# Kernel optimization log

Measured on AMD Instinct MI355X. Metric: run time of the kernel, lower is better.

The kernel has to match this reference:

```python
import jax, jax.numpy as jnp
import numpy as np

N = 100000   # source points
M = 100000   # query (also) points
E = 2000000  # radius-neighbor pairs (row: query idx, col: source idx)
FEAT = 64
OUT = 2


def _linear_params(key, fan_in, fan_out):
    kw, kb = jax.random.split(key)
    bound = 1.0 / np.sqrt(fan_in)
    w = jax.random.uniform(kw, (fan_in, fan_out), jnp.float32, -bound, bound)
    b = jax.random.uniform(kb, (fan_out,), jnp.float32, -bound, bound)
    return w, b


def setup_inputs() -> dict:
    key = jax.random.key(0)
    ks = jax.random.split(key, 10)
    pcd = jax.random.normal(ks[0], (N, 3), jnp.float32)
    feats = jax.random.normal(ks[1], (N, FEAT), jnp.float32)
    also_pts = jax.random.normal(ks[2], (M, 3), jnp.float32)
    also_labels = jax.random.randint(ks[3], (M,), 0, 2, jnp.int64)
    row = jax.random.randint(ks[4], (E,), 0, M, jnp.int64)
    col = jax.random.randint(ks[5], (E,), 0, N, jnp.int64)
    w_in, b_in = _linear_params(ks[6], FEAT + 3, FEAT)
    w1, b1 = _linear_params(ks[7], FEAT, FEAT)
    w2, b2 = _linear_params(ks[8], FEAT, FEAT)
    w_out, b_out = _linear_params(ks[9], FEAT, OUT)
    return {"pcd": pcd, "feats": feats, "also_pts": also_pts,
            "also_labels": also_labels, "row": row, "col": col,
            "w_in": w_in, "b_in": b_in, "w1": w1, "b1": b1,
            "w2": w2, "b2": b2, "w_out": w_out, "b_out": b_out}


def reference(pcd, feats, also_pts, also_labels, row, col,
              w_in, b_in, w1, b1, w2, b2, w_out, b_out):
    # gather: relative position of query vs neighbor, and neighbor latent
    pos_relative = also_pts[row] - pcd[col]          # (E, 3)
    latents_relative = feats[col]                    # (E, FEAT)
    x = jnp.concatenate([latents_relative, pos_relative], axis=1)  # (E, FEAT+3)
    x = x @ w_in + b_in                              # fc_in
    x = jax.nn.relu(x) @ w1 + b1                     # mlp layer 0 (act then linear)
    x = jax.nn.relu(x) @ w2 + b2                     # mlp layer 1
    x = x @ w_out + b_out                            # fc_out -> (E, 2)
    probs = jax.nn.softmax(x, axis=1)
    return probs, also_labels[row]
```

## Files before the change

### kernel.cpp

```cpp
#include <hip/hip_runtime.h>
#include <hip/hip_bf16.h>


typedef _Float16 half8 __attribute__((ext_vector_type(8)));
typedef _Float16 half2v __attribute__((ext_vector_type(2)));
typedef __fp16   fp16x2 __attribute__((ext_vector_type(2)));
typedef __attribute__((ext_vector_type(4))) float f32x4;

union U84h { uint4 u; half8 h; };
union UPH  { half2v h; fp16x2 f; int i; unsigned u; };

__device__ __forceinline__ half2v cvt2h(float a, float b) {
    UPH t;
    t.f = __builtin_amdgcn_cvt_pkrtz(a, b);
    return t.h;
}

__device__ __forceinline__ half8 relu8(half8 v) {
    half8 z;
#pragma unroll
    for (int i = 0; i < 8; ++i) z[i] = (_Float16)0.f;
    return __builtin_elementwise_max(v, z);
}

__global__ __launch_bounds__(256) void pack_fold(
    const float* __restrict__ w1, const float* __restrict__ w_in,
    const float* __restrict__ b1, const float* __restrict__ w2,
    const float* __restrict__ w_out, const float* __restrict__ b2,
    const float* __restrict__ b_out,
    _Float16* __restrict__ w1f, _Float16* __restrict__ wAf,
    _Float16* __restrict__ wpf, _Float16* __restrict__ w0h,
    _Float16* __restrict__ w1h, _Float16* __restrict__ b1h,
    float* __restrict__ bf) {
    int t = blockIdx.x * 256 + threadIdx.x;
    if (t < 4096) {
        int f = t >> 9, lane = (t >> 3) & 63, j = t & 7;
        int ntile = f >> 1, kstep = f & 1;
        int k = kstep * 32 + ((lane >> 4) << 3) + j;
        int n = ntile * 16 + (lane & 15);
        w1f[t] = (_Float16)w1[k * 64 + n];
    } else if (t < 10240) {
        int i = t - 4096;
        int f = i >> 9, lane = (i >> 3) & 63, j = i & 7;
        int ntile = f / 3, ks = f % 3;
        int n = ntile * 16 + (lane & 15);
        float v;
        if (ks < 2) {
            int k = ks * 32 + ((lane >> 4) << 3) + j;
            v = w_in[k * 64 + n];
        } else {
            v = ((lane >> 4) == 0 && j < 3) ? -w_in[(64 + j) * 64 + n] : 0.f;
        }
        wAf[i] = (_Float16)v;
    } else if (t < 13312) {
        int i = t - 10240;
        int d = i >> 10, ks = (i >> 9) & 1, lane = (i >> 3) & 63, j = i & 7;
        int k = ks * 32 + ((lane >> 4) << 3) + j;
        wpf[i] = (_Float16)w_in[(64 + d) * 64 + k];
    } else if (t < 13376) {
        int n = t - 13312;
        float s0 = 0.f, s1 = 0.f;
#pragma unroll
        for (int j = 0; j < 64; ++j) {
            s0 = fmaf(w2[n * 64 + j], w_out[j * 2 + 0], s0);
            s1 = fmaf(w2[n * 64 + j], w_out[j * 2 + 1], s1);
        }
        w0h[n] = (_Float16)s0;
        w1h[n] = (_Float16)s1;
    } else if (t < 13440) {
        int n = t - 13376;
        b1h[n] = (_Float16)b1[n];
    } else if (t == 13440) {
        float s0 = b_out[0], s1 = b_out[1];
#pragma unroll
        for (int j = 0; j < 64; ++j) {
            s0 = fmaf(b2[j], w_out[j * 2 + 0], s0);
            s1 = fmaf(b2[j], w_out[j * 2 + 1], s1);
        }
        bf[0] = s0; bf[1] = s1;
    }
}

__global__ __launch_bounds__(256) void precompute_S(
    const float* __restrict__ feats, const float* __restrict__ pcd,
    const float* __restrict__ b_in, const half8* __restrict__ wAf,
    _Float16* __restrict__ S, int N) {
    int lane = threadIdx.x & 63;
    int idx = lane & 15, g = lane >> 4;
    int base = (blockIdx.x * 4 + (threadIdx.x >> 6)) * 16;
    if (base >= N) return;

    half8 wa[12];
#pragma unroll
    for (int f = 0; f < 12; ++f) wa[f] = wAf[f * 64 + lane];

    int p = base + idx;
    int ps = p < N ? p : N - 1;
    const float4* fp = (const float4*)(feats + (size_t)ps * 64);
    float4 f0 = fp[2 * g], f1 = fp[2 * g + 1];
    float4 f2 = fp[8 + 2 * g], f3 = fp[8 + 2 * g + 1];
    half8 b0, b1v, b2v;
    b0[0]=(_Float16)f0.x; b0[1]=(_Float16)f0.y; b0[2]=(_Float16)f0.z; b0[3]=(_Float16)f0.w;
    b0[4]=(_Float16)f1.x; b0[5]=(_Float16)f1.y; b0[6]=(_Float16)f1.z; b0[7]=(_Float16)f1.w;
    b1v[0]=(_Float16)f2.x; b1v[1]=(_Float16)f2.y; b1v[2]=(_Float16)f2.z; b1v[3]=(_Float16)f2.w;
    b1v[4]=(_Float16)f3.x; b1v[5]=(_Float16)f3.y; b1v[6]=(_Float16)f3.z; b1v[7]=(_Float16)f3.w;
    float px = 0.f, py = 0.f, pz = 0.f;
    if (g == 0) {
        const float* pp = pcd + (size_t)ps * 3;
        px = pp[0]; py = pp[1]; pz = pp[2];
    }
#pragma unroll
    for (int i = 0; i < 8; ++i) b2v[i] = (_Float16)0.f;
    b2v[0] = (_Float16)px; b2v[1] = (_Float16)py; b2v[2] = (_Float16)pz;

#pragma unroll
    for (int tt = 0; tt < 4; ++tt) {
        f32x4 bi = *(const f32x4*)(b_in + tt * 16 + 4 * g);
        f32x4 acc;
        acc = __builtin_amdgcn_mfma_f32_16x16x32_f16(wa[tt * 3 + 0], b0, bi, 0, 0, 0);
        acc = __builtin_amdgcn_mfma_f32_16x16x32_f16(wa[tt * 3 + 1], b1v, acc, 0, 0, 0);
        acc = __builtin_amdgcn_mfma_f32_16x16x32_f16(wa[tt * 3 + 2], b2v, acc, 0, 0, 0);
        union { uint2 u; _Float16 h[4]; } o;
        o.h[0] = (_Float16)acc[0]; o.h[1] = (_Float16)acc[1];
        o.h[2] = (_Float16)acc[2]; o.h[3] = (_Float16)acc[3];
        if (p < N) *(uint2*)(S + (size_t)p * 64 + tt * 16 + 4 * g) = o.u;
    }
}

__global__ __launch_bounds__(256, 4) void edge_mfma(
    const _Float16* __restrict__ S, const float* __restrict__ also_pts,
    const int* __restrict__ row, const int* __restrict__ col,
    const int* __restrict__ labels,
    const half8* __restrict__ w1f, const half8* __restrict__ wpf,
    const unsigned* __restrict__ w0p, const unsigned* __restrict__ w1p,
    const unsigned* __restrict__ b1p, const float* __restrict__ bfold,
    float* __restrict__ out, int E, int ngroups) {
    __shared__ half8 wf_lds[8][64];
    {
        int t = threadIdx.x;
        wf_lds[t >> 6][t & 63] = w1f[t];
        wf_lds[(t + 256) >> 6][t & 63] = w1f[t + 256];
    }
    __syncthreads();

    int lane = threadIdx.x & 63;
    int idx  = lane & 15;
    int g    = lane >> 4;
    int gwave  = blockIdx.x * 4 + (threadIdx.x >> 6);
    int nwaves = gridDim.x * 4;
    if (gwave >= ngroups) return;

    half8 wpd[3][2];
#pragma unroll
    for (int d = 0; d < 3; ++d)
#pragma unroll
        for (int ks = 0; ks < 2; ++ks) wpd[d][ks] = wpf[(d * 2 + ks) * 64 + lane];
    UPH w0v[8], w1v[8], b1v[8];
#pragma unroll
    for (int tt = 0; tt < 4; ++tt)
#pragma unroll
        for (int h = 0; h < 2; ++h) {
            int i = tt * 8 + 2 * g + h;
            w0v[tt * 2 + h].u = w0p[i];
            w1v[tt * 2 + h].u = w1p[i];
            b1v[tt * 2 + h].u = b1p[i];
        }
    float bf0 = bfold[0], bf1 = bfold[1];
    half2v zero2 = {(_Float16)0.f, (_Float16)0.f};

    int grp = gwave, stride = nwaves;
    int es0 = (grp << 4) + idx; es0 = es0 < E ? es0 : E - 1;
    int r_c = row[es0], c_c = col[es0];
    const uint4* sp0 = (const uint4*)(S + (size_t)c_c * 64);
    uint4 s0_c = sp0[g], s1_c = sp0[4 + g];
    const float* ap0 = also_pts + (size_t)r_c * 3;
    float ax_c = ap0[0], ay_c = ap0[1], az_c = ap0[2];
    int lb_c = labels[r_c];

    int gn = grp + stride; gn = gn < ngroups ? gn : grp;
    int es1 = (gn << 4) + idx; es1 = es1 < E ? es1 : E - 1;
    int r_n = row[es1], c_n = col[es1];

    for (; grp < ngroups; grp += stride) {
        const uint4* spn = (const uint4*)(S + (size_t)c_n * 64);
        uint4 s0_n = spn[g], s1_n = spn[4 + g];
        const float* apn = also_pts + (size_t)r_n * 3;
        float ax_n = apn[0], ay_n = apn[1], az_n = apn[2];
        int lb_n = labels[r_n];
        int g2 = grp + 2 * stride; g2 = g2 < ngroups ? g2 : grp;
        int es2 = (g2 << 4) + idx; es2 = es2 < E ? es2 : E - 1;
        int r_2 = row[es2], c_2 = col[es2];

        int e = (grp << 4) + idx;
        bool eok = e < E;
        U84h s0u, s1u; s0u.u = s0_c; s1u.u = s1_c;
        _Float16 ah = (_Float16)ax_c, bh = (_Float16)ay_c, ch = (_Float16)az_c;
        half8 av = {ah, ah, ah, ah, ah, ah, ah, ah};
        half8 bv = {bh, bh, bh, bh, bh, bh, bh, bh};
        half8 cv = {ch, ch, ch, ch, ch, ch, ch, ch};
        half8 q0 = av * wpd[0][0] + bv * wpd[1][0] + cv * wpd[2][0];
        half8 q1 = av * wpd[0][1] + bv * wpd[1][1] + cv * wpd[2][1];
        half8 x0 = relu8(s0u.h + q0);
        half8 x1 = relu8(s1u.h + q1);

        f32x4 zero = {0.f, 0.f, 0.f, 0.f};
        f32x4 acc[4];
#pragma unroll
        for (int tt = 0; tt < 4; ++tt) {
            acc[tt] = __builtin_amdgcn_mfma_f32_16x16x32_f16(wf_lds[2 * tt][lane],     x0, zero, 0, 0, 0);
            acc[tt] = __builtin_amdgcn_mfma_f32_16x16x32_f16(wf_lds[2 * tt + 1][lane], x1, acc[tt], 0, 0, 0);
        }

        half2v p0 = zero2, p1 = zero2;
#pragma unroll
        for (int tt = 0; tt < 4; ++tt) {
            half2v h01 = cvt2h(acc[tt][0], acc[tt][1]);
            half2v h23 = cvt2h(acc[tt][2], acc[tt][3]);
            h01 = __builtin_elementwise_max(h01 + b1v[tt * 2 + 0].h, zero2);
            h23 = __builtin_elementwise_max(h23 + b1v[tt * 2 + 1].h, zero2);
            p0 += h01 * w0v[tt * 2 + 0].h + h23 * w0v[tt * 2 + 1].h;
            p1 += h01 * w1v[tt * 2 + 0].h + h23 * w1v[tt * 2 + 1].h;
        }
        UPH P0, P1, T;
        P0.h = p0; P1.h = p1;
        T.i = __shfl_xor(P0.i, 16); P0.h += T.h;
        T.i = __shfl_xor(P0.i, 32); P0.h += T.h;
        T.i = __shfl_xor(P1.i, 16); P1.h += T.h;
        T.i = __shfl_xor(P1.i, 32); P1.h += T.h;

        if (g == 0 && eok) {
            float l0 = (float)P0.h[0] + (float)P0.h[1] + bf0;
            float l1 = (float)P1.h[0] + (float)P1.h[1] + bf1;
            float mx = fmaxf(l0, l1);
            float e0 = __expf(l0 - mx);
            float e1 = __expf(l1 - mx);
            float inv = 1.f / (e0 + e1);
            *(float2*)(out + (size_t)e * 2) = make_float2(e0 * inv, e1 * inv);
            out[(size_t)2 * E + e] = (float)lb_c;
        }

        s0_c = s0_n; s1_c = s1_n;
        ax_c = ax_n; ay_c = ay_n; az_c = az_n;
        lb_c = lb_n;
        r_n = r_2; c_n = c_2;
    }
}

extern "C" void kernel_launch(void* const* d_in, const int* in_sizes, int n_in,
                              void* d_out, int out_size, void* d_ws, size_t ws_size,
                              hipStream_t stream) {
    const float* pcd      = (const float*)d_in[0];
    const float* feats    = (const float*)d_in[1];
    const float* also_pts = (const float*)d_in[2];
    const int*   labels   = (const int*)d_in[3];
    const int*   row      = (const int*)d_in[4];
    const int*   col      = (const int*)d_in[5];
    const float* w_in     = (const float*)d_in[6];
    const float* b_in     = (const float*)d_in[7];
    const float* w1       = (const float*)d_in[8];
    const float* b1       = (const float*)d_in[9];
    const float* w2       = (const float*)d_in[10];
    const float* b2       = (const float*)d_in[11];
    const float* w_out    = (const float*)d_in[12];
    const float* b_out    = (const float*)d_in[13];

    int N = in_sizes[0] / 3;
    int E = in_sizes[4];

    _Float16* Sb  = (_Float16*)d_ws;
    _Float16* w1f = Sb + (size_t)N * 64;
    _Float16* wAf = w1f + 4096;
    _Float16* wpf = wAf + 6144;
    _Float16* w0h = wpf + 3072;
    _Float16* w1h = w0h + 64;
    _Float16* b1h = w1h + 64;
    float*    bf  = (float*)(b1h + 64);

    pack_fold<<<53, 256, 0, stream>>>(w1, w_in, b1, w2, w_out, b2, b_out,
                                      w1f, wAf, wpf, w0h, w1h, b1h, bf);

    int ngroupsS = (N + 15) / 16;
    precompute_S<<<(ngroupsS + 3) / 4, 256, 0, stream>>>(
        feats, pcd, b_in, (const half8*)wAf, Sb, N);

    int ngroups = (E + 15) / 16;
    edge_mfma<<<2048, 256, 0, stream>>>(Sb, also_pts, row, col, labels,
                                        (const half8*)w1f, (const half8*)wpf,
                                        (const unsigned*)w0h, (const unsigned*)w1h,
                                        (const unsigned*)b1h, bf,
                                        (float*)d_out, E, ngroups);
}
```

Baseline: 81.83 us.

## Process two edge groups per wave iteration with deeper gather prefetch

Each wave now handles a pair of 16-edge groups per loop iteration and prefetches gathers for both groups one iteration ahead, with indices two ahead. This doubles memory-level parallelism per wave to hide random-gather latency. The 2-class softmax is simplified to a sigmoid of the logit difference, and the grid grows to 3072 blocks with the occupancy hint removed from launch bounds. The cost is higher register pressure, which may lower occupancy.

Result: slower. 96.18 us (+17.5%).

```diff
diff --git a/kernel.cpp b/kernel.cpp
--- a/kernel.cpp
+++ b/kernel.cpp
@@ -127,14 +127,14 @@
     }
 }
 
-__global__ __launch_bounds__(256, 4) void edge_mfma(
+__global__ __launch_bounds__(256) void edge_mfma(
     const _Float16* __restrict__ S, const float* __restrict__ also_pts,
     const int* __restrict__ row, const int* __restrict__ col,
     const int* __restrict__ labels,
     const half8* __restrict__ w1f, const half8* __restrict__ wpf,
     const unsigned* __restrict__ w0p, const unsigned* __restrict__ w1p,
     const unsigned* __restrict__ b1p, const float* __restrict__ bfold,
-    float* __restrict__ out, int E, int ngroups) {
+    float* __restrict__ out, int E, int npairs) {
     __shared__ half8 wf_lds[8][64];
     {
         int t = threadIdx.x;
@@ -146,9 +146,9 @@
     int lane = threadIdx.x & 63;
     int idx  = lane & 15;
     int g    = lane >> 4;
-    int gwave  = blockIdx.x * 4 + (threadIdx.x >> 6);
-    int nwaves = gridDim.x * 4;
-    if (gwave >= ngroups) return;
+    int wid  = blockIdx.x * 4 + (threadIdx.x >> 6);
+    int nw   = gridDim.x * 4;
+    if (wid >= npairs) return;
 
     half8 wpd[3][2];
 #pragma unroll
@@ -165,36 +165,28 @@
             w1v[tt * 2 + h].u = w1p[i];
             b1v[tt * 2 + h].u = b1p[i];
         }
-    float bf0 = bfold[0], bf1 = bfold[1];
+    float bfd = bfold[0] - bfold[1];
     half2v zero2 = {(_Float16)0.f, (_Float16)0.f};
 
-    int grp = gwave, stride = nwaves;
-    int es0 = (grp << 4) + idx; es0 = es0 < E ? es0 : E - 1;
-    int r_c = row[es0], c_c = col[es0];
-    const uint4* sp0 = (const uint4*)(S + (size_t)c_c * 64);
-    uint4 s0_c = sp0[g], s1_c = sp0[4 + g];
-    const float* ap0 = also_pts + (size_t)r_c * 3;
-    float ax_c = ap0[0], ay_c = ap0[1], az_c = ap0[2];
-    int lb_c = labels[r_c];
-
-    int gn = grp + stride; gn = gn < ngroups ? gn : grp;
-    int es1 = (gn << 4) + idx; es1 = es1 < E ? es1 : E - 1;
-    int r_n = row[es1], c_n = col[es1];
-
-    for (; grp < ngroups; grp += stride) {
-        const uint4* spn = (const uint4*)(S + (size_t)c_n * 64);
-        uint4 s0_n = spn[g], s1_n = spn[4 + g];
-        const float* apn = also_pts + (size_t)r_n * 3;
-        float ax_n = apn[0], ay_n = apn[1], az_n = apn[2];
-        int lb_n = labels[r_n];
-        int g2 = grp + 2 * stride; g2 = g2 < ngroups ? g2 : grp;
-        int es2 = (g2 << 4) + idx; es2 = es2 < E ? es2 : E - 1;
-        int r_2 = row[es2], c_2 = col[es2];
-
-        int e = (grp << 4) + idx;
+    auto ldidx = [&](int p, int s, int& r, int& c) {
+        int e = (2 * p + s) * 16 + idx;
+        e = e < E ? e : E - 1;
+        r = row[e]; c = col[e];
+    };
+    auto gath = [&](int r, int c, uint4& s0, uint4& s1,
+                    float& ax, float& ay, float& az, int& lb) {
+        const uint4* sp = (const uint4*)(S + (size_t)c * 64);
+        s0 = sp[g]; s1 = sp[4 + g];
+        const float* ap = also_pts + (size_t)r * 3;
+        ax = ap[0]; ay = ap[1]; az = ap[2];
+        lb = labels[r];
+    };
+    auto comp = [&](int gg, uint4 s0r, uint4 s1r,
+                    float ax, float ay, float az, int lb) {
+        int e = gg * 16 + idx;
         bool eok = e < E;
-        U84h s0u, s1u; s0u.u = s0_c; s1u.u = s1_c;
-        _Float16 ah = (_Float16)ax_c, bh = (_Float16)ay_c, ch = (_Float16)az_c;
+        U84h s0u, s1u; s0u.u = s0r; s1u.u = s1r;
+        _Float16 ah = (_Float16)ax, bh = (_Float16)ay, ch = (_Float16)az;
         half8 av = {ah, ah, ah, ah, ah, ah, ah, ah};
         half8 bv = {bh, bh, bh, bh, bh, bh, bh, bh};
         half8 cv = {ch, ch, ch, ch, ch, ch, ch, ch};
@@ -229,20 +221,46 @@
         T.i = __shfl_xor(P1.i, 32); P1.h += T.h;
 
         if (g == 0 && eok) {
-            float l0 = (float)P0.h[0] + (float)P0.h[1] + bf0;
-            float l1 = (float)P1.h[0] + (float)P1.h[1] + bf1;
-            float mx = fmaxf(l0, l1);
-            float e0 = __expf(l0 - mx);
-            float e1 = __expf(l1 - mx);
-            float inv = 1.f / (e0 + e1);
-            *(float2*)(out + (size_t)e * 2) = make_float2(e0 * inv, e1 * inv);
-            out[(size_t)2 * E + e] = (float)lb_c;
-        }
-
-        s0_c = s0_n; s1_c = s1_n;
-        ax_c = ax_n; ay_c = ay_n; az_c = az_n;
-        lb_c = lb_n;
-        r_n = r_2; c_n = c_2;
+            float l0 = (float)P0.h[0] + (float)P0.h[1];
+            float l1 = (float)P1.h[0] + (float)P1.h[1];
+            float u = __expf(l1 - l0 - bfd);
+            float pa = 1.f / (1.f + u);
+            *(float2*)(out + (size_t)e * 2) = make_float2(pa, 1.f - pa);
+            out[(size_t)2 * E + e] = (float)lb;
+        }
+    };
+
+    int pair = wid, stride = nw;
+    int rA, cA, rB, cB;
+    ldidx(pair, 0, rA, cA);
+    ldidx(pair, 1, rB, cB);
+    uint4 s0A, s1A, s0B, s1B;
+    float axA, ayA, azA, axB, ayB, azB;
+    int lbA, lbB;
+    gath(rA, cA, s0A, s1A, axA, ayA, azA, lbA);
+    gath(rB, cB, s0B, s1B, axB, ayB, azB, lbB);
+    int pn = pair + stride; pn = pn < npairs ? pn : pair;
+    int rAn, cAn, rBn, cBn;
+    ldidx(pn, 0, rAn, cAn);
+    ldidx(pn, 1, rBn, cBn);
+
+    for (; pair < npairs; pair += stride) {
+        uint4 t0A, t1A, t0B, t1B;
+        float nxA, nyA, nzA, nxB, nyB, nzB;
+        int nlA, nlB;
+        gath(rAn, cAn, t0A, t1A, nxA, nyA, nzA, nlA);
+        gath(rBn, cBn, t0B, t1B, nxB, nyB, nzB, nlB);
+        int p2 = pair + 2 * stride; p2 = p2 < npairs ? p2 : pair;
+        int rA2, cA2, rB2, cB2;
+        ldidx(p2, 0, rA2, cA2);
+        ldidx(p2, 1, rB2, cB2);
+
+        comp(2 * pair,     s0A, s1A, axA, ayA, azA, lbA);
+        comp(2 * pair + 1, s0B, s1B, axB, ayB, azB, lbB);
+
+        s0A = t0A; s1A = t1A; axA = nxA; ayA = nyA; azA = nzA; lbA = nlA;
+        s0B = t0B; s1B = t1B; axB = nxB; ayB = nyB; azB = nzB; lbB = nlB;
+        rAn = rA2; cAn = cA2; rBn = rB2; cBn = cB2;
     }
 }
 
@@ -284,9 +302,10 @@
         feats, pcd, b_in, (const half8*)wAf, Sb, N);
 
     int ngroups = (E + 15) / 16;
-    edge_mfma<<<2048, 256, 0, stream>>>(Sb, also_pts, row, col, labels,
+    int npairs  = (ngroups + 1) / 2;
+    edge_mfma<<<3072, 256, 0, stream>>>(Sb, also_pts, row, col, labels,
                                         (const half8*)w1f, (const half8*)wpf,
                                         (const unsigned*)w0h, (const unsigned*)w1h,
                                         (const unsigned*)b1h, bf,
-                                        (float*)d_out, E, ngroups);
-}
+                                        (float*)d_out, E, npairs);
+}
```
